# Kernel tuning notes

Hardware: AMD Instinct MI355X
Metric: run time of the kernel (lower is better)

## Reference

```python
import jax, jax.numpy as jnp
import numpy as np
from jax import lax

NL, DM, DI, DS, DTR, NC = 4, 128, 256, 16, 8, 256  # layers, d_model, d_inner, d_state, dt_rank, classes
B, L = 24, 3072  # conv stride 3 -> T = 1024


def _ln(x, w, b, eps=1e-5):
    mu = x.mean(-1, keepdims=True)
    v = ((x - mu) ** 2).mean(-1, keepdims=True)
    return (x - mu) * lax.rsqrt(v + eps) * w + b


def _mixer(h, inp, cw, cb, xp, dtw, dtb, Alog, D):
    # h: (B,T,DM) -> Mamba selective-scan mixer output (B,T,DI) before out_proj
    xz = h @ inp.T                                   # (B,T,2*DI)
    x, z = jnp.split(xz, 2, axis=-1)
    # causal depthwise conv (torch pads d_conv-1=3 both sides then slices [:T] == left-pad 3)
    xc = lax.conv_general_dilated(x.transpose(0, 2, 1), cw, (1,), [(3, 0)],
                                  feature_group_count=DI,
                                  dimension_numbers=('NCH', 'OIH', 'NCH'))
    xc = jax.nn.silu((xc + cb[None, :, None]).transpose(0, 2, 1))   # (B,T,DI)
    dbl = xc @ xp.T                                  # (B,T,DTR+2*DS)
    dt = jax.nn.softplus(dbl[..., :DTR] @ dtw.T + dtb)              # (B,T,DI)
    Bm, Cm = dbl[..., DTR:DTR + DS], dbl[..., DTR + DS:]            # (B,T,DS) each
    A = -jnp.exp(Alog)                               # (DI,DS)

    def step(hst, ins):
        dt_t, B_t, C_t, x_t = ins                    # (B,DI),(B,DS),(B,DS),(B,DI)
        hst = jnp.exp(dt_t[..., None] * A) * hst + (dt_t * x_t)[..., None] * B_t[:, None, :]
        return hst, jnp.einsum('bds,bs->bd', hst, C_t)

    h0 = jnp.zeros((h.shape[0], DI, DS), h.dtype)
    xs = (dt.transpose(1, 0, 2), Bm.transpose(1, 0, 2), Cm.transpose(1, 0, 2), xc.transpose(1, 0, 2))
    _, ys = lax.scan(step, h0, xs)                   # ys: (T,B,DI)
    y = ys.transpose(1, 0, 2) + D * xc
    return y * jax.nn.silu(z)


def _stack(h, p, nf_w, nf_b):
    residual = None
    for i in range(NL):
        residual = h if residual is None else h + residual
        hn = _ln(residual, p['lnw'][i], p['lnb'][i])
        y = _mixer(hn, p['inp'][i], p['cw'][i], p['cb'][i], p['xp'][i],
                   p['dtw'][i], p['dtb'][i], p['Alog'][i], p['D'][i])
        h = y @ p['outp'][i].T
    return _ln(h + residual, nf_w, nf_b)


def _forward(x, conv_w, conv_b, fp, bp, nf_w, nf_b, head_w, head_b):
    c = lax.conv_general_dilated(x[:, None, :], conv_w, (3,), [(1, 1)],
                                 dimension_numbers=('NCH', 'OIH', 'NCH'))
    h = (c + conv_b[None, :, None]).transpose(0, 2, 1)   # (B,T,DM)
    fw = _stack(h, fp, nf_w, nf_b)
    bw = _stack(h[:, ::-1, :], bp, nf_w, nf_b)
    comb = jnp.concatenate([fw[:, -1, :], bw[:, -1, :]], axis=-1)  # (B,2*DM)
    return comb @ head_w.T + head_b


def setup_inputs():
    key = jax.random.key(0)
    ks = iter(jax.random.split(key, 64))

    def rn(shape, s):
        return jax.random.normal(next(ks), shape, jnp.float32) * s

    def layer(prefix):
        dt0 = jnp.clip(jax.random.uniform(next(ks), (NL, DI)) * 0.1, 1e-3, None)
        return {
            prefix + '_inp': rn((NL, 2 * DI, DM), 0.05),
            prefix + '_cw': rn((NL, DI, 1, 4), 0.3),
            prefix + '_cb': rn((NL, DI), 0.02),
            prefix + '_xp': rn((NL, DTR + 2 * DS, DI), 0.05),
            prefix + '_dtw': rn((NL, DI, DTR), 0.1),
            prefix + '_dtb': jnp.log(jnp.expm1(dt0)),  # inverse-softplus of small positive dt
            prefix + '_Alog': jnp.log(jnp.broadcast_to(jnp.arange(1, DS + 1, dtype=jnp.float32), (NL, DI, DS))),
            prefix + '_D': jnp.ones((NL, DI), jnp.float32),
            prefix + '_outp': rn((NL, DM, DI), 0.05),
            prefix + '_lnw': jnp.ones((NL, DM), jnp.float32),
            prefix + '_lnb': jnp.zeros((NL, DM), jnp.float32),
        }

    inp = {'x': rn((B, L), 1.0), 'conv_w': rn((DM, 1, 3), 0.3), 'conv_b': jnp.zeros((DM,), jnp.float32)}
    inp.update(layer('f'))
    inp.update(layer('b'))
    inp.update({'nf_w': jnp.ones((DM,), jnp.float32), 'nf_b': jnp.zeros((DM,), jnp.float32),
                'head_w': rn((NC, 2 * DM), 0.05), 'head_b': jnp.zeros((NC,), jnp.float32)})
    return inp


def reference(x, conv_w, conv_b,
              f_inp, f_cw, f_cb, f_xp, f_dtw, f_dtb, f_Alog, f_D, f_outp, f_lnw, f_lnb,
              b_inp, b_cw, b_cb, b_xp, b_dtw, b_dtb, b_Alog, b_D, b_outp, b_lnw, b_lnb,
              nf_w, nf_b, head_w, head_b):
    fp = dict(inp=f_inp, cw=f_cw, cb=f_cb, xp=f_xp, dtw=f_dtw, dtb=f_dtb,
              Alog=f_Alog, D=f_D, outp=f_outp, lnw=f_lnw, lnb=f_lnb)
    bp = dict(inp=b_inp, cw=b_cw, cb=b_cb, xp=b_xp, dtw=b_dtw, dtb=b_dtb,
              Alog=b_Alog, D=b_D, outp=b_outp, lnw=b_lnw, lnb=b_lnb)
    return _forward(x, conv_w, conv_b, fp, bp, nf_w, nf_b, head_w, head_b)
```

## Files before the change

### kernel.cpp

```cpp
#include <hip/hip_runtime.h>
#include <hip/hip_bf16.h>
#include <math.h>

static constexpr int NL=4, DM=128, DI=256, DS=16, DTR=8, NC=256;
static constexpr int Bb=24, Lx=3072, T=1024;
static constexpr int ROWS = Bb*T;
static constexpr int NCH=8, TC=128;

typedef __attribute__((ext_vector_type(4))) float f32x4;
typedef __attribute__((ext_vector_type(8))) short bf16x8;

static __device__ inline unsigned short f2bf(float f){
  unsigned int u = __float_as_uint(f);
  unsigned int r = (u + 0x7FFFu + ((u >> 16) & 1u)) >> 16;
  return (unsigned short)r;
}

template<int CTRL>
static __device__ __forceinline__ float dpp_add(float x){
  int t = __builtin_amdgcn_update_dpp(0, __float_as_int(x), CTRL, 0xF, 0xF, true);
  return x + __int_as_float(t);
}

__global__ __launch_bounds__(256) void k_conv0(const float* __restrict__ x,
    const float* __restrict__ cw, const float* __restrict__ cb,
    float* __restrict__ h0f, float* __restrict__ h0b){
  int idx = blockIdx.x*256 + threadIdx.x;
  int c = idx & (DM-1);
  int t = (idx >> 7) & (T-1);
  int b = idx >> 17;
  const float* xr = x + b*Lx;
  float acc = cb[c];
  int base = 3*t - 1;
#pragma unroll
  for (int k=0;k<3;k++){
    int j = base + k;
    float xv = (j>=0 && j<Lx) ? xr[j] : 0.f;
    acc = fmaf(xv, cw[c*3+k], acc);
  }
  h0f[(b*T + t)*DM + c] = acc;
  h0b[(b*T + (T-1-t))*DM + c] = acc;
}

__global__ __launch_bounds__(256) void k_cast(const float* __restrict__ src,
    unsigned short* __restrict__ dst, int n){
  int i = blockIdx.x*256 + threadIdx.x;
  if (i < n) dst[i] = f2bf(src[i]);
}

__global__ __launch_bounds__(256) void k_add_ln(const float* __restrict__ hin,
    float* __restrict__ res, const float* __restrict__ lnw, const float* __restrict__ lnb,
    unsigned short* __restrict__ hn, int first){
  int row = blockIdx.x*4 + (threadIdx.x >> 6);
  int lane = threadIdx.x & 63;
  const float* hr = hin + (long)row*DM;
  float* rr = res + (long)row*DM;
  float v0 = hr[lane], v1 = hr[lane+64];
  if (!first){ v0 += rr[lane]; v1 += rr[lane+64]; }
  rr[lane] = v0; rr[lane+64] = v1;
  float s = v0+v1;
#pragma unroll
  for (int m=1;m<64;m<<=1) s += __shfl_xor(s, m);
  float mu = s * (1.f/128.f);
  float d0 = v0-mu, d1 = v1-mu;
  float q = d0*d0 + d1*d1;
#pragma unroll
  for (int m=1;m<64;m<<=1) q += __shfl_xor(q, m);
  float rstd = rsqrtf(q*(1.f/128.f) + 1e-5f);
  hn[(long)row*DM+lane]    = f2bf(d0*rstd*lnw[lane]    + lnb[lane]);
  hn[(long)row*DM+lane+64] = f2bf(d1*rstd*lnw[lane+64] + lnb[lane+64]);
}

template<int N, int K>
__global__ __launch_bounds__(256) void k_mgemm(const unsigned short* __restrict__ A,
    const unsigned short* __restrict__ W, float* __restrict__ C){
  constexpr int BK = 32;
  __shared__ short As[128*BK];
  __shared__ short Ws[128*BK];
  int tid = threadIdx.x;
  int lane = tid & 63, wave = tid >> 6;
  int wr = (wave >> 1) * 64, wc = (wave & 1) * 64;
  long bm = blockIdx.x, bn = blockIdx.y;
  const short* Ag = (const short*)A + bm*128*K;
  const short* Wg = (const short*)W + bn*128*K;
  f32x4 acc[4][4] = {};
  int r = lane & 15, kg = (lane >> 4) * 8;
  for (int kb = 0; kb < K; kb += BK){
#pragma unroll
    for (int t = 0; t < 2; t++){
      int c = tid + t*256;
      int row = c >> 2, kc = (c & 3) * 8;
      *(bf16x8*)&As[row*BK + kc] = *(const bf16x8*)&Ag[row*K + kb + kc];
      *(bf16x8*)&Ws[row*BK + kc] = *(const bf16x8*)&Wg[row*K + kb + kc];
    }
    __syncthreads();
    bf16x8 af[4], wf[4];
#pragma unroll
    for (int m=0;m<4;m++) af[m] = *(const bf16x8*)&As[(wr + m*16 + r)*BK + kg];
#pragma unroll
    for (int n=0;n<4;n++) wf[n] = *(const bf16x8*)&Ws[(wc + n*16 + r)*BK + kg];
#pragma unroll
    for (int m=0;m<4;m++)
#pragma unroll
      for (int n=0;n<4;n++)
        acc[m][n] = __builtin_amdgcn_mfma_f32_16x16x32_bf16(af[m], wf[n], acc[m][n], 0, 0, 0);
    __syncthreads();
  }
  float* Cb = C + (bm*128)*N + bn*128;
  int rq = (lane >> 4) * 4, cn = lane & 15;
#pragma unroll
  for (int m=0;m<4;m++)
#pragma unroll
    for (int n=0;n<4;n++)
#pragma unroll
      for (int q=0;q<4;q++)
        Cb[(wr + m*16 + rq + q)*N + wc + n*16 + cn] = acc[m][n][q];
}

__global__ __launch_bounds__(256) void k_convs(const float* __restrict__ xz,
    const float* __restrict__ cw, const float* __restrict__ cb,
    float* __restrict__ xc, unsigned short* __restrict__ xcb){
  int idx = blockIdx.x*256 + threadIdx.x;
  int d = idx & (DI-1);
  int t = (idx >> 8) & (T-1);
  int b = idx >> 18;
  const float* xrow = xz + (long)b*T*2*DI;
  float acc = cb[d];
#pragma unroll
  for (int k=0;k<4;k++){
    int tt = t + k - 3;
    float xv = (tt>=0) ? xrow[(long)tt*2*DI + d] : 0.f;
    acc = fmaf(xv, cw[d*4+k], acc);
  }
  float s = acc / (1.f + __expf(-acc));
  long o = (long)(b*T+t)*DI + d;
  xc[o] = s;
  xcb[o] = f2bf(s);
}

__global__ __launch_bounds__(256) void k_dbldt(const unsigned short* __restrict__ xcb,
    const unsigned short* __restrict__ xpb, const float* __restrict__ dtw,
    const float* __restrict__ dtb, float* __restrict__ gdt, float* __restrict__ bcg){
  constexpr int BP = 264;
  __shared__ short B_s[48*BP];
  __shared__ float dbl_s[64][9];
  __shared__ float bc_s[64][33];
  int tid = threadIdx.x;
  int lane = tid & 63, wave = tid >> 6;
  int wr = wave * 16;
  long row0 = (long)blockIdx.x * 64;
  float w[8];
#pragma unroll
  for (int j=0;j<8;j++) w[j] = dtw[tid*8 + j];
  float bias = dtb[tid];
  for (int c = tid; c < 48*32; c += 256){
    int rowp = c >> 5, k8 = (c & 31) * 8;
    bf16x8 v = {};
    if (rowp < 40) v = *(const bf16x8*)&xpb[rowp*256 + k8];
    *(bf16x8*)&B_s[rowp*BP + k8] = v;
  }
  __syncthreads();
  int cf = lane & 15, hi = lane >> 4;
  const short* Ag = (const short*)xcb + (row0 + wr + cf)*DI + hi*8;
  f32x4 acc[3] = {};
#pragma unroll
  for (int ks = 0; ks < 8; ks++){
    bf16x8 af = *(const bf16x8*)&Ag[ks*32];
#pragma unroll
    for (int n = 0; n < 3; n++){
      bf16x8 bf = *(const bf16x8*)&B_s[(n*16 + cf)*BP + ks*32 + hi*8];
      acc[n] = __builtin_amdgcn_mfma_f32_16x16x32_bf16(af, bf, acc[n], 0, 0, 0);
    }
  }
#pragma unroll
  for (int n = 0; n < 3; n++){
    int col = n*16 + cf;
#pragma unroll
    for (int q = 0; q < 4; q++){
      int row = wr + hi*4 + q;
      float v = acc[n][q];
      if (col < 8)       dbl_s[row][col]    = v;
      else if (col < 40) bc_s[row][col - 8] = v;
    }
  }
  __syncthreads();
#pragma unroll
  for (int i = 0; i < 8; i++){
    int idx = tid + i*256;
    int row = idx >> 5, col = idx & 31;
    bcg[(row0 + row)*32 + col] = bc_s[row][col];
  }
  for (int r = 0; r < 64; r++){
    float a = bias;
#pragma unroll
    for (int j = 0; j < 8; j++) a = fmaf(dbl_s[r][j], w[j], a);
    float sp = (a > 20.f) ? a : log1pf(__expf(a));
    gdt[(row0 + r)*DI + tid] = sp;
  }
}

__global__ __launch_bounds__(256) void k_scan1(const float* __restrict__ gdt,
    const float* __restrict__ bcg, const float* __restrict__ xc,
    const float* __restrict__ Alog, float* __restrict__ Pd, float* __restrict__ Hl){
  int b = blockIdx.z, ch = blockIdx.y, d0 = blockIdx.x*16;
  int tid = threadIdx.x, s = tid & 15, dl = tid >> 4, d = d0 + dl;
  float A = -__expf(Alog[d*DS + s]);
  __shared__ float dt_s[TC][16], x_s[TC][16], b_s[TC][16];
  long r0 = (long)b*T + ch*TC;
  for (int lin = tid; lin < TC*4; lin += 256){
    int i = lin >> 2, c4 = (lin & 3)*4;
    *(float4*)&dt_s[i][c4] = *(const float4*)&gdt[(r0+i)*DI + d0 + c4];
    *(float4*)&x_s[i][c4]  = *(const float4*)&xc [(r0+i)*DI + d0 + c4];
    *(float4*)&b_s[i][c4]  = *(const float4*)&bcg[(r0+i)*32 + c4];
  }
  __syncthreads();
  float h = 0.f, lp = 0.f;
  for (int i0 = 0; i0 < TC; i0 += 8){
    float dtv[8], xv[8], bv[8];
#pragma unroll
    for (int j=0;j<8;j++){ dtv[j]=dt_s[i0+j][dl]; xv[j]=x_s[i0+j][dl]; bv[j]=b_s[i0+j][s]; }
#pragma unroll
    for (int j=0;j<8;j++){
      float da = dtv[j]*A;
      lp += da;
      h = fmaf(__expf(da), h, dtv[j]*xv[j]*bv[j]);
    }
  }
  long o = ((long)(b*NCH + ch)*DI + d)*DS + s;
  Pd[o] = __expf(lp);
  Hl[o] = h;
}

__global__ __launch_bounds__(256) void k_scan2(const float* __restrict__ Pd,
    const float* __restrict__ Hl, float* __restrict__ Hst){
  int idx = blockIdx.x*256 + threadIdx.x;
  int b = idx >> 12, j = idx & 4095;
  long base = (long)b*NCH*4096 + j;
  float h = 0.f;
#pragma unroll
  for (int c=0;c<NCH;c++){
    Hst[base + c*4096] = h;
    h = Pd[base + c*4096]*h + Hl[base + c*4096];
  }
}

__global__ __launch_bounds__(256) void k_scan3(const float* __restrict__ gdt,
    const float* __restrict__ bcg, const float* __restrict__ xc, const float* __restrict__ xz,
    const float* __restrict__ Alog, const float* __restrict__ Dp,
    const float* __restrict__ Hst, unsigned short* __restrict__ yg){
  int b = blockIdx.z, ch = blockIdx.y, d0 = blockIdx.x*16;
  int tid = threadIdx.x, s = tid & 15, dl = tid >> 4, d = d0 + dl;
  float A = -__expf(Alog[d*DS + s]);
  float Dd = Dp[d];
  __shared__ float dt_s[TC][16], x_s[TC][16], z_s[TC][16], b_s[TC][16], c_s[TC][16];
  __shared__ float y_s[TC][16];
  long r0 = (long)b*T + ch*TC;
  for (int lin = tid; lin < TC*4; lin += 256){
    int i = lin >> 2, c4 = (lin & 3)*4;
    *(float4*)&dt_s[i][c4] = *(const float4*)&gdt[(r0+i)*DI + d0 + c4];
    *(float4*)&x_s[i][c4]  = *(const float4*)&xc [(r0+i)*DI + d0 + c4];
    float4 zv = *(const float4*)&xz [(r0+i)*2*DI + DI + d0 + c4];
    zv.x = zv.x/(1.f+__expf(-zv.x)); zv.y = zv.y/(1.f+__expf(-zv.y));
    zv.z = zv.z/(1.f+__expf(-zv.z)); zv.w = zv.w/(1.f+__expf(-zv.w));
    *(float4*)&z_s[i][c4]  = zv;
    *(float4*)&b_s[i][c4]  = *(const float4*)&bcg[(r0+i)*32 + c4];
    *(float4*)&c_s[i][c4]  = *(const float4*)&bcg[(r0+i)*32 + 16 + c4];
  }
  float h = Hst[((long)(b*NCH + ch)*DI + d)*DS + s];
  __syncthreads();
  for (int i0 = 0; i0 < TC; i0 += 8){
    float dtv[8], xv[8], bv[8], cv[8], dec[8], ad[8], p[8];
#pragma unroll
    for (int j=0;j<8;j++){
      dtv[j]=dt_s[i0+j][dl]; xv[j]=x_s[i0+j][dl];
      bv[j]=b_s[i0+j][s];    cv[j]=c_s[i0+j][s];
    }
#pragma unroll
    for (int j=0;j<8;j++){ dec[j] = __expf(dtv[j]*A); ad[j] = dtv[j]*xv[j]*bv[j]; }
#pragma unroll
    for (int j=0;j<8;j++){ h = fmaf(dec[j], h, ad[j]); p[j] = h * cv[j]; }
#pragma unroll
    for (int j=0;j<8;j++) p[j] = dpp_add<0xB1>(p[j]);
#pragma unroll
    for (int j=0;j<8;j++) p[j] = dpp_add<0x4E>(p[j]);
#pragma unroll
    for (int j=0;j<8;j++) p[j] = dpp_add<0x114>(p[j]);
#pragma unroll
    for (int j=0;j<8;j++) p[j] = dpp_add<0x118>(p[j]);
    if (s == 0){
#pragma unroll
      for (int j=0;j<8;j++)
        y_s[i0+j][dl] = fmaf(Dd, xv[j], p[j]) * z_s[i0+j][dl];
    }
  }
  __syncthreads();
  for (int lin = tid; lin < TC*2; lin += 256){
    int i = lin >> 1, dd8 = (lin & 1)*8;
    bf16x8 v;
#pragma unroll
    for (int k=0;k<8;k++) v[k] = (short)f2bf(y_s[i][dd8+k]);
    *(bf16x8*)&yg[(r0+i)*DI + d0 + dd8] = v;
  }
}

__global__ __launch_bounds__(64) void k_final(const float* __restrict__ hcur,
    const float* __restrict__ res, const float* __restrict__ nfw, const float* __restrict__ nfb,
    float* __restrict__ comb, int half){
  int b = blockIdx.x;
  int lane = threadIdx.x;
  const float* h = hcur + ((long)b*T + (T-1))*DM;
  const float* r = res  + ((long)b*T + (T-1))*DM;
  float v0 = h[lane]+r[lane], v1 = h[lane+64]+r[lane+64];
  float s = v0+v1;
#pragma unroll
  for (int m=1;m<64;m<<=1) s += __shfl_xor(s, m);
  float mu = s * (1.f/128.f);
  float d0 = v0-mu, d1 = v1-mu;
  float q = d0*d0 + d1*d1;
#pragma unroll
  for (int m=1;m<64;m<<=1) q += __shfl_xor(q, m);
  float rstd = rsqrtf(q*(1.f/128.f) + 1e-5f);
  comb[b*2*DM + half*DM + lane]    = d0*rstd*nfw[lane]    + nfb[lane];
  comb[b*2*DM + half*DM + lane+64] = d1*rstd*nfw[lane+64] + nfb[lane+64];
}

__global__ __launch_bounds__(256) void k_head(const float* __restrict__ comb,
    const float* __restrict__ hw, const float* __restrict__ hb, float* __restrict__ out){
  int b = blockIdx.x, n = threadIdx.x;
  const float* cr = comb + b*2*DM;
  float acc = hb[n];
#pragma unroll 4
  for (int k=0;k<2*DM;k++) acc = fmaf(cr[k], hw[n*2*DM + k], acc);
  out[b*NC + n] = acc;
}

extern "C" void kernel_launch(void* const* d_in, const int* in_sizes, int n_in,
                              void* d_out, int out_size, void* d_ws, size_t ws_size,
                              hipStream_t stream){
  auto F = [&](int i){ return (const float*)d_in[i]; };
  float* ws = (float*)d_ws;
  size_t o = 0;
  float* h0f = ws + o; o += (size_t)ROWS*DM;
  float* h0b = ws + o; o += (size_t)ROWS*DM;
  float* res = ws + o; o += (size_t)ROWS*DM;
  float* hcur= ws + o; o += (size_t)ROWS*DM;
  float* xz  = ws + o; o += (size_t)ROWS*2*DI;
  float* xc  = ws + o; o += (size_t)ROWS*DI;
  float* gdt = ws + o; o += (size_t)ROWS*DI;
  float* bcg = ws + o; o += (size_t)ROWS*2*DS;
  unsigned short* ybf = (unsigned short*)(ws + o); o += (size_t)ROWS*DI/2;
  unsigned short* hnbf = ybf;
  unsigned short* xcb  = ybf;
  float* Pd  = ws + o; o += (size_t)Bb*NCH*DI*DS;
  float* Hl  = ws + o; o += (size_t)Bb*NCH*DI*DS;
  float* Hst = ws + o; o += (size_t)Bb*NCH*DI*DS;
  unsigned short* wbf = (unsigned short*)(ws + o); o += (size_t)2*NL*(2*DI*DM + DM*DI)/2;
  unsigned short* xpb = (unsigned short*)(ws + o); o += (size_t)2*NL*40*DI/2;
  float* comb= ws + o; o += (size_t)Bb*2*DM;

  const int NI = NL*2*DI*DM;
  const int NO = NL*DM*DI;
  const int NX = NL*40*DI;
  k_cast<<<(NI+255)/256, 256, 0, stream>>>(F(3),  wbf,            NI);
  k_cast<<<(NO+255)/256, 256, 0, stream>>>(F(11), wbf+NI,         NO);
  k_cast<<<(NI+255)/256, 256, 0, stream>>>(F(14), wbf+NI+NO,      NI);
  k_cast<<<(NO+255)/256, 256, 0, stream>>>(F(22), wbf+2*NI+NO,    NO);
  k_cast<<<(NX+255)/256, 256, 0, stream>>>(F(6),  xpb,            NX);
  k_cast<<<(NX+255)/256, 256, 0, stream>>>(F(17), xpb+NX,         NX);

  k_conv0<<<ROWS*DM/256, 256, 0, stream>>>(F(0), F(1), F(2), h0f, h0b);

  for (int dir = 0; dir < 2; dir++){
    int p = dir ? 14 : 3;
    const float* hin = dir ? h0b : h0f;
    unsigned short* winp  = wbf + (size_t)dir*(NI+NO);
    unsigned short* woutp = winp + NI;
    for (int l = 0; l < NL; l++){
      const float* hsrc = (l==0) ? hin : hcur;
      k_add_ln<<<ROWS/4, 256, 0, stream>>>(hsrc, res,
          F(p+9)+(size_t)l*DM, F(p+10)+(size_t)l*DM, hnbf, (l==0)?1:0);
      k_mgemm<2*DI, DM><<<dim3(ROWS/128, (2*DI)/128), 256, 0, stream>>>(
          hnbf, winp + (size_t)l*2*DI*DM, xz);
      k_convs<<<ROWS*DI/256, 256, 0, stream>>>(xz,
          F(p+1)+(size_t)l*DI*4, F(p+2)+(size_t)l*DI, xc, xcb);
      k_dbldt<<<ROWS/64, 256, 0, stream>>>(xcb,
          xpb + (size_t)(dir*NL + l)*40*DI,
          F(p+4)+(size_t)l*DI*DTR, F(p+5)+(size_t)l*DI, gdt, bcg);
      k_scan1<<<dim3(DI/16, NCH, Bb), 256, 0, stream>>>(gdt, bcg, xc,
          F(p+6)+(size_t)l*DI*DS, Pd, Hl);
      k_scan2<<<(Bb*DI*DS)/256, 256, 0, stream>>>(Pd, Hl, Hst);
      k_scan3<<<dim3(DI/16, NCH, Bb), 256, 0, stream>>>(gdt, bcg, xc, xz,
          F(p+6)+(size_t)l*DI*DS, F(p+7)+(size_t)l*DI, Hst, ybf);
      k_mgemm<DM, DI><<<dim3(ROWS/128, DM/128), 256, 0, stream>>>(
          ybf, woutp + (size_t)l*DM*DI, hcur);
    }
    k_final<<<Bb, 64, 0, stream>>>(hcur, res, F(25), F(26), comb, dir);
  }
  k_head<<<Bb, 256, 0, stream>>>(comb, F(27), F(28), (float*)d_out);
}
```

Before: 1.578 ms.

## Read scan inputs directly from global and use 64-row tiles for out_proj GEMM

The scan kernels stop staging dt, x, z, B and C chunks in shared memory and instead read them per step straight from global memory through cached loads. This drops the prologue copy and barrier and frees LDS for more blocks per CU, but makes each access a strided global load that depends on cache hits. Separately, the out_proj GEMM (N=128) gets a 64-row tile variant so it launches twice as many blocks and fills more CUs.

```diff
diff --git a/kernel.cpp b/kernel.cpp
--- a/kernel.cpp
+++ b/kernel.cpp
@@ -117,6 +117,56 @@
         Cb[(wr + m*16 + rq + q)*N + wc + n*16 + cn] = acc[m][n][q];
 }
 
+template<int N, int K>
+__global__ __launch_bounds__(256) void k_mgemm64(const unsigned short* __restrict__ A,
+    const unsigned short* __restrict__ W, float* __restrict__ C){
+  constexpr int BK = 32;
+  __shared__ short As[64*BK];
+  __shared__ short Ws[128*BK];
+  int tid = threadIdx.x;
+  int lane = tid & 63, wave = tid >> 6;
+  int wr = (wave >> 1) * 32, wc = (wave & 1) * 64;
+  long bm = blockIdx.x, bn = blockIdx.y;
+  const short* Ag = (const short*)A + bm*64*K;
+  const short* Wg = (const short*)W + bn*128*K;
+  f32x4 acc[2][4] = {};
+  int r = lane & 15, kg = (lane >> 4) * 8;
+  for (int kb = 0; kb < K; kb += BK){
+    {
+      int c = tid;
+      int row = c >> 2, kc = (c & 3) * 8;
+      *(bf16x8*)&As[row*BK + kc] = *(const bf16x8*)&Ag[row*K + kb + kc];
+#pragma unroll
+      for (int t = 0; t < 2; t++){
+        int c2 = tid + t*256;
+        int row2 = c2 >> 2, kc2 = (c2 & 3) * 8;
+        *(bf16x8*)&Ws[row2*BK + kc2] = *(const bf16x8*)&Wg[row2*K + kb + kc2];
+      }
+    }
+    __syncthreads();
+    bf16x8 af[2], wf[4];
+#pragma unroll
+    for (int m=0;m<2;m++) af[m] = *(const bf16x8*)&As[(wr + m*16 + r)*BK + kg];
+#pragma unroll
+    for (int n=0;n<4;n++) wf[n] = *(const bf16x8*)&Ws[(wc + n*16 + r)*BK + kg];
+#pragma unroll
+    for (int m=0;m<2;m++)
+#pragma unroll
+      for (int n=0;n<4;n++)
+        acc[m][n] = __builtin_amdgcn_mfma_f32_16x16x32_bf16(af[m], wf[n], acc[m][n], 0, 0, 0);
+    __syncthreads();
+  }
+  float* Cb = C + (bm*64)*N + bn*128;
+  int rq = (lane >> 4) * 4, cn = lane & 15;
+#pragma unroll
+  for (int m=0;m<2;m++)
+#pragma unroll
+    for (int n=0;n<4;n++)
+#pragma unroll
+      for (int q=0;q<4;q++)
+        Cb[(wr + m*16 + rq + q)*N + wc + n*16 + cn] = acc[m][n][q];
+}
+
 __global__ __launch_bounds__(256) void k_convs(const float* __restrict__ xz,
     const float* __restrict__ cw, const float* __restrict__ cb,
     float* __restrict__ xc, unsigned short* __restrict__ xcb){
@@ -205,20 +255,19 @@
   int b = blockIdx.z, ch = blockIdx.y, d0 = blockIdx.x*16;
   int tid = threadIdx.x, s = tid & 15, dl = tid >> 4, d = d0 + dl;
   float A = -__expf(Alog[d*DS + s]);
-  __shared__ float dt_s[TC][16], x_s[TC][16], b_s[TC][16];
   long r0 = (long)b*T + ch*TC;
-  for (int lin = tid; lin < TC*4; lin += 256){
-    int i = lin >> 2, c4 = (lin & 3)*4;
-    *(float4*)&dt_s[i][c4] = *(const float4*)&gdt[(r0+i)*DI + d0 + c4];
-    *(float4*)&x_s[i][c4]  = *(const float4*)&xc [(r0+i)*DI + d0 + c4];
-    *(float4*)&b_s[i][c4]  = *(const float4*)&bcg[(r0+i)*32 + c4];
-  }
-  __syncthreads();
+  const float* gdt_p = gdt + r0*DI + d;
+  const float* xc_p  = xc  + r0*DI + d;
+  const float* b_p   = bcg + r0*32 + s;
   float h = 0.f, lp = 0.f;
   for (int i0 = 0; i0 < TC; i0 += 8){
     float dtv[8], xv[8], bv[8];
 #pragma unroll
-    for (int j=0;j<8;j++){ dtv[j]=dt_s[i0+j][dl]; xv[j]=x_s[i0+j][dl]; bv[j]=b_s[i0+j][s]; }
+    for (int j=0;j<8;j++){
+      dtv[j] = gdt_p[(i0+j)*DI];
+      xv[j]  = xc_p [(i0+j)*DI];
+      bv[j]  = b_p  [(i0+j)*32];
+    }
 #pragma unroll
     for (int j=0;j<8;j++){
       float da = dtv[j]*A;
@@ -252,28 +301,22 @@
   int tid = threadIdx.x, s = tid & 15, dl = tid >> 4, d = d0 + dl;
   float A = -__expf(Alog[d*DS + s]);
   float Dd = Dp[d];
-  __shared__ float dt_s[TC][16], x_s[TC][16], z_s[TC][16], b_s[TC][16], c_s[TC][16];
   __shared__ float y_s[TC][16];
   long r0 = (long)b*T + ch*TC;
-  for (int lin = tid; lin < TC*4; lin += 256){
-    int i = lin >> 2, c4 = (lin & 3)*4;
-    *(float4*)&dt_s[i][c4] = *(const float4*)&gdt[(r0+i)*DI + d0 + c4];
-    *(float4*)&x_s[i][c4]  = *(const float4*)&xc [(r0+i)*DI + d0 + c4];
-    float4 zv = *(const float4*)&xz [(r0+i)*2*DI + DI + d0 + c4];
-    zv.x = zv.x/(1.f+__expf(-zv.x)); zv.y = zv.y/(1.f+__expf(-zv.y));
-    zv.z = zv.z/(1.f+__expf(-zv.z)); zv.w = zv.w/(1.f+__expf(-zv.w));
-    *(float4*)&z_s[i][c4]  = zv;
-    *(float4*)&b_s[i][c4]  = *(const float4*)&bcg[(r0+i)*32 + c4];
-    *(float4*)&c_s[i][c4]  = *(const float4*)&bcg[(r0+i)*32 + 16 + c4];
-  }
+  const float* gdt_p = gdt + r0*DI + d;
+  const float* xc_p  = xc  + r0*DI + d;
+  const float* z_p   = xz  + r0*2*DI + DI + d;
+  const float* b_p   = bcg + r0*32 + s;
+  const float* c_p   = b_p + 16;
   float h = Hst[((long)(b*NCH + ch)*DI + d)*DS + s];
-  __syncthreads();
   for (int i0 = 0; i0 < TC; i0 += 8){
     float dtv[8], xv[8], bv[8], cv[8], dec[8], ad[8], p[8];
 #pragma unroll
     for (int j=0;j<8;j++){
-      dtv[j]=dt_s[i0+j][dl]; xv[j]=x_s[i0+j][dl];
-      bv[j]=b_s[i0+j][s];    cv[j]=c_s[i0+j][s];
+      dtv[j] = gdt_p[(i0+j)*DI];
+      xv[j]  = xc_p [(i0+j)*DI];
+      bv[j]  = b_p  [(i0+j)*32];
+      cv[j]  = c_p  [(i0+j)*32];
     }
 #pragma unroll
     for (int j=0;j<8;j++){ dec[j] = __expf(dtv[j]*A); ad[j] = dtv[j]*xv[j]*bv[j]; }
@@ -289,8 +332,11 @@
     for (int j=0;j<8;j++) p[j] = dpp_add<0x118>(p[j]);
     if (s == 0){
 #pragma unroll
-      for (int j=0;j<8;j++)
-        y_s[i0+j][dl] = fmaf(Dd, xv[j], p[j]) * z_s[i0+j][dl];
+      for (int j=0;j<8;j++){
+        float zv = z_p[(i0+j)*2*DI];
+        float sz = zv / (1.f + __expf(-zv));
+        y_s[i0+j][dl] = fmaf(Dd, xv[j], p[j]) * sz;
+      }
     }
   }
   __syncthreads();
@@ -391,7 +437,7 @@
       k_scan2<<<(Bb*DI*DS)/256, 256, 0, stream>>>(Pd, Hl, Hst);
       k_scan3<<<dim3(DI/16, NCH, Bb), 256, 0, stream>>>(gdt, bcg, xc, xz,
           F(p+6)+(size_t)l*DI*DS, F(p+7)+(size_t)l*DI, Hst, ybf);
-      k_mgemm<DM, DI><<<dim3(ROWS/128, DM/128), 256, 0, stream>>>(
+      k_mgemm64<DM, DI><<<dim3(ROWS/64, DM/128), 256, 0, stream>>>(
           ybf, woutp + (size_t)l*DM*DI, hcur);
     }
     k_final<<<Bb, 64, 0, stream>>>(hcur, res, F(25), F(26), comb, dir);
```

New measurement: 1.896 ms. 20.2% more time.
